# Kernel tuning notes

Hardware: AMD Instinct MI355X
Metric: run time of the kernel (lower is better)

The kernel has to match this reference:

```python
import jax, jax.numpy as jnp
import numpy as np

STRIDE = (16, 16)
PADDING = (0, 0)


def setup_inputs() -> dict:
    key = jax.random.key(0)
    k1, k2, k3 = jax.random.split(key, 3)
    x = jax.random.normal(k1, (16, 12, 512, 512), dtype=jnp.float32)
    weight = jax.random.normal(k2, (768, 1, 16, 16), dtype=jnp.float32) * 0.02
    bias = jax.random.normal(k3, (768,), dtype=jnp.float32) * 0.02
    return {"x": x, "weight": weight, "bias": bias}


def reference(x, weight, bias):
    # Faithful to the torch module: groups=c conv with the shared filter
    # repeated per input channel, then mean over the channel axis, then bias.
    b, c, h, w = x.shape
    o = weight.shape[0]
    # groups=c conv with repeated weight == independent conv of each channel
    # with the same (o,1,kh,kw) filter; fold channels into batch.
    xc = x.reshape(b * c, 1, h, w)
    y = jax.lax.conv_general_dilated(
        xc, weight,
        window_strides=STRIDE,
        padding=[(PADDING[0], PADDING[0]), (PADDING[1], PADDING[1])],
        dimension_numbers=("NCHW", "OIHW", "NCHW"),
    )  # (b*c, o, H', W')
    hp, wp = y.shape[-2], y.shape[-1]
    y = y.reshape(b, c, o, hp, wp).mean(axis=1)  # (b, o, H', W')
    y = y + bias[None, :, None, None]
    return y
```

## Files before the change

kernel.cpp:

```cpp
#include <hip/hip_runtime.h>
#include <hip/hip_bf16.h>

#define BATCH 16
#define CIN   12
#define HIMG  512
#define WIMG  512
#define OCH   768
#define KDIM  256
#define HW    (HIMG*WIMG)
#define NPATCH 1024

#define MEAN_BLOCKS 4096
#define PACK_BLOCKS 96

typedef __attribute__((ext_vector_type(8))) short short8;
typedef __attribute__((ext_vector_type(4))) float f32x4;

__global__ __launch_bounds__(256) void mean_pack_kernel(
        const float* __restrict__ x, __hip_bfloat16* __restrict__ xm,
        const float* __restrict__ w, short8* __restrict__ wbp) {
    const int bid = blockIdx.x;
    if (bid < MEAN_BLOCKS) {
        int idx = bid * 256 + threadIdx.x;
        int b = idx >> 16;
        int pos = (idx & 65535) << 2;
        const float* px = x + (size_t)b * CIN * HW + pos;
        float sx = 0.f, sy = 0.f, sz = 0.f, sw = 0.f;
        #pragma unroll
        for (int c = 0; c < CIN; ++c) {
            f32x4 v = *reinterpret_cast<const f32x4*>(px + (size_t)c * HW);
            sx += v.x; sy += v.y; sz += v.z; sw += v.w;
        }
        const float inv = 1.0f / 12.0f;
        union { ushort4 u4; __hip_bfloat16 h[4]; } o;
        o.h[0] = __float2bfloat16(sx * inv);
        o.h[1] = __float2bfloat16(sy * inv);
        o.h[2] = __float2bfloat16(sz * inv);
        o.h[3] = __float2bfloat16(sw * inv);
        *reinterpret_cast<ushort4*>(xm + (size_t)idx * 4) = o.u4;
    } else {
        int u = (bid - MEAN_BLOCKS) * 256 + threadIdx.x;
        int lane = u & 63;
        int kk   = (u >> 6) & 7;
        int ot   = u >> 9;
        int o = ot * 16 + (lane & 15);
        int k = kk * 32 + (lane >> 4) * 8;
        const float* src = w + (size_t)o * KDIM + k;
        f32x4 v0 = *reinterpret_cast<const f32x4*>(src);
        f32x4 v1 = *reinterpret_cast<const f32x4*>(src + 4);
        union { short8 s; __hip_bfloat16 h[8]; } t;
        t.h[0] = __float2bfloat16(v0.x);
        t.h[1] = __float2bfloat16(v0.y);
        t.h[2] = __float2bfloat16(v0.z);
        t.h[3] = __float2bfloat16(v0.w);
        t.h[4] = __float2bfloat16(v1.x);
        t.h[5] = __float2bfloat16(v1.y);
        t.h[6] = __float2bfloat16(v1.z);
        t.h[7] = __float2bfloat16(v1.w);
        wbp[u] = t.s;
    }
}

__global__ __launch_bounds__(512, 4) void gemm_kernel(
        const short8* __restrict__ wbp,
        const __hip_bfloat16* __restrict__ xm,
        const float* __restrict__ bias,
        float* __restrict__ out) {
    const int tid = threadIdx.x;
    const int b  = blockIdx.x >> 5;
    const int sp = (blockIdx.x >> 1) & 15;
    const int oh = blockIdx.x & 1;

    const int lane = tid & 63;
    const int wv   = tid >> 6;
    const int lrow = lane & 15;
    const int lg   = lane >> 4;

    const __hip_bfloat16* xmb = xm + (size_t)b * HW + sp * (32 * WIMG)
                                + (lg >> 1) * WIMG + (lg & 1) * 8;
    int e0[4];
    #pragma unroll
    for (int fm = 0; fm < 4; ++fm) {
        const int ml = fm * 16 + lrow;
        e0[fm] = (ml >> 5) * (16 * WIMG) + (ml & 31) * 16;
    }

    f32x4 acc[3][4] = {};
    const short8* wp = wbp + (size_t)(oh * 24 + wv * 3) * 8 * 64 + lane;

    #pragma unroll
    for (int kk = 0; kk < 8; ++kk) {
        short8 af[3], bf[4];
        #pragma unroll
        for (int fo = 0; fo < 3; ++fo)
            af[fo] = wp[(size_t)(fo * 8 + kk) * 64];
        #pragma unroll
        for (int fm = 0; fm < 4; ++fm)
            bf[fm] = *reinterpret_cast<const short8*>(xmb + e0[fm] + kk * (2 * WIMG));
        #pragma unroll
        for (int fo = 0; fo < 3; ++fo)
            #pragma unroll
            for (int fm = 0; fm < 4; ++fm)
                acc[fo][fm] = __builtin_amdgcn_mfma_f32_16x16x32_bf16(af[fo], bf[fm], acc[fo][fm], 0, 0, 0);
    }

    float* ob = out + (size_t)b * OCH * NPATCH + sp * 64;
    #pragma unroll
    for (int fo = 0; fo < 3; ++fo) {
        const int obase = oh * 384 + wv * 48 + fo * 16 + lg * 4;
        #pragma unroll
        for (int r = 0; r < 4; ++r) {
            const int o = obase + r;
            const float bv = bias[o];
            float* orow = ob + (size_t)o * NPATCH;
            #pragma unroll
            for (int fm = 0; fm < 4; ++fm)
                orow[fm * 16 + lrow] = acc[fo][fm][r] + bv;
        }
    }
}

extern "C" void kernel_launch(void* const* d_in, const int* in_sizes, int n_in,
                              void* d_out, int out_size, void* d_ws, size_t ws_size,
                              hipStream_t stream) {
    const float* x    = (const float*)d_in[0];
    const float* w    = (const float*)d_in[1];
    const float* bias = (const float*)d_in[2];
    float* out = (float*)d_out;

    __hip_bfloat16* xm = (__hip_bfloat16*)d_ws;
    short8* wbp = (short8*)((char*)d_ws + (size_t)BATCH * HW * 2);

    mean_pack_kernel<<<MEAN_BLOCKS + PACK_BLOCKS, 256, 0, stream>>>(x, xm, w, wbp);
    gemm_kernel<<<512, 512, 0, stream>>>(wbp, xm, bias, out);
}
```

Before: 51.53 us.

## Split batch in halves to overlap GEMM of first half with mean of second

Splits the channel-mean reduction and the bf16 GEMM into two batch halves across three launches, so the GEMM for the first half runs in the same grid as the mean for the second half. GEMM blocks shrink to 256 threads and each covers a quarter of the output channels. The aim is to hide GEMM time under the memory-bound mean pass. It adds a third kernel launch and mixes compute blocks with bandwidth-heavy blocks, which may contend with each other.

Measured after the change: 55.53 us. 7.8% more time.

```diff
diff --git a/kernel.cpp b/kernel.cpp
--- a/kernel.cpp
+++ b/kernel.cpp
@@ -10,66 +10,61 @@
 #define HW    (HIMG*WIMG)
 #define NPATCH 1024
 
-#define MEAN_BLOCKS 4096
-#define PACK_BLOCKS 96
-
 typedef __attribute__((ext_vector_type(8))) short short8;
 typedef __attribute__((ext_vector_type(4))) float f32x4;
 
-__global__ __launch_bounds__(256) void mean_pack_kernel(
-        const float* __restrict__ x, __hip_bfloat16* __restrict__ xm,
-        const float* __restrict__ w, short8* __restrict__ wbp) {
-    const int bid = blockIdx.x;
-    if (bid < MEAN_BLOCKS) {
-        int idx = bid * 256 + threadIdx.x;
-        int b = idx >> 16;
-        int pos = (idx & 65535) << 2;
-        const float* px = x + (size_t)b * CIN * HW + pos;
-        float sx = 0.f, sy = 0.f, sz = 0.f, sw = 0.f;
-        #pragma unroll
-        for (int c = 0; c < CIN; ++c) {
-            f32x4 v = *reinterpret_cast<const f32x4*>(px + (size_t)c * HW);
-            sx += v.x; sy += v.y; sz += v.z; sw += v.w;
-        }
-        const float inv = 1.0f / 12.0f;
-        union { ushort4 u4; __hip_bfloat16 h[4]; } o;
-        o.h[0] = __float2bfloat16(sx * inv);
-        o.h[1] = __float2bfloat16(sy * inv);
-        o.h[2] = __float2bfloat16(sz * inv);
-        o.h[3] = __float2bfloat16(sw * inv);
-        *reinterpret_cast<ushort4*>(xm + (size_t)idx * 4) = o.u4;
-    } else {
-        int u = (bid - MEAN_BLOCKS) * 256 + threadIdx.x;
-        int lane = u & 63;
-        int kk   = (u >> 6) & 7;
-        int ot   = u >> 9;
-        int o = ot * 16 + (lane & 15);
-        int k = kk * 32 + (lane >> 4) * 8;
-        const float* src = w + (size_t)o * KDIM + k;
-        f32x4 v0 = *reinterpret_cast<const f32x4*>(src);
-        f32x4 v1 = *reinterpret_cast<const f32x4*>(src + 4);
-        union { short8 s; __hip_bfloat16 h[8]; } t;
-        t.h[0] = __float2bfloat16(v0.x);
-        t.h[1] = __float2bfloat16(v0.y);
-        t.h[2] = __float2bfloat16(v0.z);
-        t.h[3] = __float2bfloat16(v0.w);
-        t.h[4] = __float2bfloat16(v1.x);
-        t.h[5] = __float2bfloat16(v1.y);
-        t.h[6] = __float2bfloat16(v1.z);
-        t.h[7] = __float2bfloat16(v1.w);
-        wbp[u] = t.s;
+__device__ __forceinline__ void mean_body(int local_bid, int tid, int hb,
+                                          const float* __restrict__ x,
+                                          __hip_bfloat16* __restrict__ xm) {
+    int idx = local_bid * 256 + tid;
+    int b = hb * 8 + (idx >> 16);
+    int pos = (idx & 65535) << 2;
+    const float* px = x + (size_t)b * CIN * HW + pos;
+    float sx = 0.f, sy = 0.f, sz = 0.f, sw = 0.f;
+    #pragma unroll
+    for (int c = 0; c < CIN; ++c) {
+        f32x4 v = *reinterpret_cast<const f32x4*>(px + (size_t)c * HW);
+        sx += v.x; sy += v.y; sz += v.z; sw += v.w;
     }
+    const float inv = 1.0f / 12.0f;
+    union { ushort4 u4; __hip_bfloat16 h[4]; } o;
+    o.h[0] = __float2bfloat16(sx * inv);
+    o.h[1] = __float2bfloat16(sy * inv);
+    o.h[2] = __float2bfloat16(sz * inv);
+    o.h[3] = __float2bfloat16(sw * inv);
+    *reinterpret_cast<ushort4*>(xm + (size_t)b * HW + pos) = o.u4;
 }
 
-__global__ __launch_bounds__(512, 4) void gemm_kernel(
-        const short8* __restrict__ wbp,
-        const __hip_bfloat16* __restrict__ xm,
-        const float* __restrict__ bias,
-        float* __restrict__ out) {
-    const int tid = threadIdx.x;
-    const int b  = blockIdx.x >> 5;
-    const int sp = (blockIdx.x >> 1) & 15;
-    const int oh = blockIdx.x & 1;
+__device__ __forceinline__ void pack_body(int u, const float* __restrict__ w,
+                                          short8* __restrict__ wbp) {
+    int lane = u & 63;
+    int kk   = (u >> 6) & 7;
+    int ot   = u >> 9;
+    int o = ot * 16 + (lane & 15);
+    int k = kk * 32 + (lane >> 4) * 8;
+    const float* src = w + (size_t)o * KDIM + k;
+    f32x4 v0 = *reinterpret_cast<const f32x4*>(src);
+    f32x4 v1 = *reinterpret_cast<const f32x4*>(src + 4);
+    union { short8 s; __hip_bfloat16 h[8]; } t;
+    t.h[0] = __float2bfloat16(v0.x);
+    t.h[1] = __float2bfloat16(v0.y);
+    t.h[2] = __float2bfloat16(v0.z);
+    t.h[3] = __float2bfloat16(v0.w);
+    t.h[4] = __float2bfloat16(v1.x);
+    t.h[5] = __float2bfloat16(v1.y);
+    t.h[6] = __float2bfloat16(v1.z);
+    t.h[7] = __float2bfloat16(v1.w);
+    wbp[u] = t.s;
+}
+
+__device__ __forceinline__ void gemm_body(int gid, int tid, int hb,
+                                          const short8* __restrict__ wbp,
+                                          const __hip_bfloat16* __restrict__ xm,
+                                          const float* __restrict__ bias,
+                                          float* __restrict__ out) {
+    const int oq = gid & 3;
+    const int sp = (gid >> 2) & 15;
+    const int b  = hb * 8 + (gid >> 6);
 
     const int lane = tid & 63;
     const int wv   = tid >> 6;
@@ -86,7 +81,7 @@
     }
 
     f32x4 acc[3][4] = {};
-    const short8* wp = wbp + (size_t)(oh * 24 + wv * 3) * 8 * 64 + lane;
+    const short8* wp = wbp + (size_t)(oq * 12 + wv * 3) * 8 * 64 + lane;
 
     #pragma unroll
     for (int kk = 0; kk < 8; ++kk) {
@@ -107,7 +102,7 @@
     float* ob = out + (size_t)b * OCH * NPATCH + sp * 64;
     #pragma unroll
     for (int fo = 0; fo < 3; ++fo) {
-        const int obase = oh * 384 + wv * 48 + fo * 16 + lg * 4;
+        const int obase = oq * 192 + wv * 48 + fo * 16 + lg * 4;
         #pragma unroll
         for (int r = 0; r < 4; ++r) {
             const int o = obase + r;
@@ -118,6 +113,29 @@
                 orow[fm * 16 + lrow] = acc[fo][fm][r] + bv;
         }
     }
+}
+
+__global__ __launch_bounds__(256) void k1_kernel(
+        const float* __restrict__ x, __hip_bfloat16* __restrict__ xm,
+        const float* __restrict__ w, short8* __restrict__ wbp) {
+    const int bid = blockIdx.x;
+    if (bid < 2048) mean_body(bid, threadIdx.x, 0, x, xm);
+    else            pack_body((bid - 2048) * 256 + threadIdx.x, w, wbp);
+}
+
+__global__ __launch_bounds__(256) void k2_kernel(
+        const float* __restrict__ x, __hip_bfloat16* __restrict__ xm,
+        const short8* __restrict__ wbp, const float* __restrict__ bias,
+        float* __restrict__ out) {
+    const int bid = blockIdx.x;
+    if (bid < 512) gemm_body(bid, threadIdx.x, 0, wbp, xm, bias, out);
+    else           mean_body(bid - 512, threadIdx.x, 1, x, xm);
+}
+
+__global__ __launch_bounds__(256) void k3_kernel(
+        const short8* __restrict__ wbp, const __hip_bfloat16* __restrict__ xm,
+        const float* __restrict__ bias, float* __restrict__ out) {
+    gemm_body(blockIdx.x, threadIdx.x, 1, wbp, xm, bias, out);
 }
 
 extern "C" void kernel_launch(void* const* d_in, const int* in_sizes, int n_in,
@@ -131,6 +149,7 @@
     __hip_bfloat16* xm = (__hip_bfloat16*)d_ws;
     short8* wbp = (short8*)((char*)d_ws + (size_t)BATCH * HW * 2);
 
-    mean_pack_kernel<<<MEAN_BLOCKS + PACK_BLOCKS, 256, 0, stream>>>(x, xm, w, wbp);
-    gemm_kernel<<<512, 512, 0, stream>>>(wbp, xm, bias, out);
+    k1_kernel<<<2144, 256, 0, stream>>>(x, xm, w, wbp);
+    k2_kernel<<<2560, 256, 0, stream>>>(x, xm, wbp, bias, out);
+    k3_kernel<<<512,  256, 0, stream>>>(wbp, xm, bias, out);
 }
```
